# Kernel tuning notes

Hardware: AMD Instinct MI355X
Metric: run time of the kernel (lower is better)

## Reference

```python
import jax, jax.numpy as jnp
import numpy as np

N = 50000        # n_nodes
E = 800000       # n_edges (avg degree 16)
H = 64           # hidden_size
ALPHA = 0.5      # CRF alpha
BETA = 0.5       # CRF beta
N_LAYER = 2      # args.crf_layer
GAMMA = 0.2      # LeakyReLU negative slope


def setup_inputs() -> dict:
    key = jax.random.key(0)
    k = jax.random.split(key, 5)
    emb = jax.random.normal(k[0], (N, H), jnp.float32)
    W_fc = jax.random.normal(k[1], (H, H), jnp.float32) / np.sqrt(H)
    attn_fc_w = jax.random.normal(k[2], (1, 2 * H), jnp.float32) / np.sqrt(2 * H)
    src = jax.random.randint(k[3], (E,), 0, N, dtype=jnp.int32)
    dst = jax.random.randint(k[4], (E,), 0, N, dtype=jnp.int32)
    return {"emb": emb, "W_fc": W_fc, "attn_fc_w": attn_fc_w, "src": src, "dst": dst}


def _segment_softmax(e, dst, n):
    # softmax over incoming edges of each destination node (DGL mailbox softmax)
    m = jax.ops.segment_max(e, dst, num_segments=n)
    m = jnp.where(jnp.isfinite(m), m, 0.0)  # nodes with no in-edges
    ex = jnp.exp(e - m[dst])
    denom = jax.ops.segment_sum(ex, dst, num_segments=n)
    return ex / jnp.maximum(denom[dst], 1e-16)


def reference(emb, W_fc, attn_fc_w, src, dst):
    # attn_fc(concat(z_src, z_dst)) split into two per-node projections
    a_src = attn_fc_w[0, :H]
    a_dst = attn_fc_w[0, H:]
    h = emb
    e = None
    for _ in range(N_LAYER):
        z = h @ W_fc.T                              # [N, H] emb_attn
        e = (z @ a_src)[src] + (z @ a_dst)[dst]     # [E] edge logits
        e = jnp.where(e > 0, e, GAMMA * e)          # LeakyReLU(gamma)
        att = _segment_softmax(e, dst, N)           # [E]
        crf = jax.ops.segment_sum(att[:, None] * h[src], dst, num_segments=N)  # [N, H]
        h = (ALPHA * emb + BETA * crf) / (ALPHA + BETA)
    # training loss (is_train=True); reuses last layer's edge logits e
    loss_a = jnp.sum((h - emb) ** 2, axis=-1)                     # [N]
    att = _segment_softmax(e, dst, N)
    diff = jnp.sqrt(jnp.sum((h[dst] - h[src]) ** 2, axis=-1) + 1e-12)  # [E] L2 norm
    loss_b = jax.ops.segment_sum(att * diff, dst, num_segments=N)  # [N]
    loss = jnp.mean(ALPHA * loss_a + BETA * loss_b)
    return h, loss
```

## Files before the change

kernel.cpp:

```cpp
#include <hip/hip_runtime.h>

#define NNODES 50000
#define NEDGES 800000
#define HDIM 64
#define CAP 64
#define GAMMA 0.2f
#define INIT_B 256
#define INIT_NB ((NNODES + INIT_B - 1) / INIT_B)
#define NPART 8
#define NODES_PER_PART ((NNODES + NPART - 1) / NPART)
#define FILL_SLICES 192
#define E4 (NEDGES / 4)
#define CHUNK ((E4 + FILL_SLICES - 1) / FILL_SLICES)
#define NB ((NNODES + 3) / 4)

typedef unsigned short u16;
typedef unsigned int u32;

__device__ __forceinline__ u16 f2bf(float f) {
    u32 u = __float_as_uint(f);
    u32 r = (u + 0x7FFFu + ((u >> 16) & 1u)) >> 16;
    return (u16)r;
}
__device__ __forceinline__ float bflo(u32 u) { return __uint_as_float(u << 16); }
__device__ __forceinline__ float bfhi(u32 u) { return __uint_as_float(u & 0xFFFF0000u); }

__device__ __forceinline__ float wave_sum(float v) {
    #pragma unroll
    for (int off = 32; off; off >>= 1) v += __shfl_xor(v, off, 64);
    return v;
}
__device__ __forceinline__ float wave_max(float v) {
    #pragma unroll
    for (int off = 32; off; off >>= 1) v = fmaxf(v, __shfl_xor(v, off, 64));
    return v;
}
__device__ __forceinline__ float group8_sum(float v) {
    v += __shfl_xor(v, 1, 64);
    v += __shfl_xor(v, 2, 64);
    v += __shfl_xor(v, 4, 64);
    return v;
}

__global__ __launch_bounds__(256) void k_init(int* __restrict__ cursor,
                                              const float* __restrict__ Wfc,
                                              const float* __restrict__ attn,
                                              float* __restrict__ ws, float* __restrict__ wd) {
    int t = threadIdx.x;
    int idx = blockIdx.x * 256 + t;
    if (idx < NNODES) cursor[idx] = 0;
    if (blockIdx.x == gridDim.x - 1) {
        if (t >= 128) {
            int tt = t - 128;
            int k = tt & 63;
            const float* av = attn + ((tt >= 64) ? HDIM : 0);
            float s = 0.f;
            for (int j = 0; j < HDIM; ++j) s += Wfc[j * HDIM + k] * av[j];
            if (tt < 64) ws[k] = s; else wd[k] = s;
        }
    }
}

__global__ __launch_bounds__(256) void k_fillx(const int4* __restrict__ src4,
                                               const int4* __restrict__ dst4,
                                               int* __restrict__ cursor,
                                               u16* __restrict__ padded,
                                               const float* __restrict__ emb,
                                               const float* __restrict__ ws,
                                               const float* __restrict__ wd,
                                               u16* __restrict__ emb_bf,
                                               float* __restrict__ zs,
                                               float* __restrict__ zd) {
    const int part = blockIdx.x & (NPART - 1);
    const int slice = blockIdx.x >> 3;
    const int lo = slice * CHUNK;
    const int hi = min(lo + CHUNK, E4);
    const int plo = part * NODES_PER_PART;
    const int phi = plo + NODES_PER_PART;
    for (int i = lo + threadIdx.x; i < hi; i += 256) {
        int4 d = dst4[i];
        bool mx = d.x >= plo && d.x < phi;
        bool my = d.y >= plo && d.y < phi;
        bool mz = d.z >= plo && d.z < phi;
        bool mw = d.w >= plo && d.w < phi;
        if (mx | my | mz | mw) {
            int4 s = src4[i];
            if (mx) { int p0 = atomicAdd(&cursor[d.x], 1); if (p0 < CAP) padded[d.x * CAP + p0] = (u16)s.x; }
            if (my) { int p1 = atomicAdd(&cursor[d.y], 1); if (p1 < CAP) padded[d.y * CAP + p1] = (u16)s.y; }
            if (mz) { int p2 = atomicAdd(&cursor[d.z], 1); if (p2 < CAP) padded[d.z * CAP + p2] = (u16)s.z; }
            if (mw) { int p3 = atomicAdd(&cursor[d.w], 1); if (p3 < CAP) padded[d.w * CAP + p3] = (u16)s.w; }
        }
    }
    const int lane = threadIdx.x & 63;
    const int gw = (blockIdx.x * 256 + threadIdx.x) >> 6;
    const int nw = (gridDim.x * 256) >> 6;
    const float wsl = ws[lane], wdl = wd[lane];
    for (int n = gw; n < NNODES; n += nw) {
        float v = emb[n * HDIM + lane];
        emb_bf[n * HDIM + lane] = f2bf(v);
        float a = wave_sum(v * wsl);
        float b = wave_sum(v * wdl);
        if (lane == 0) { zs[n] = a; zd[n] = b; }
    }
}

template <bool COMPUTE_Z, bool WRITE_F32, bool STORE_LA>
__global__ __launch_bounds__(256) void k_layer(const u16* __restrict__ hbf_in,
                                               const float* __restrict__ emb,
                                               const int* __restrict__ deg,
                                               const u16* __restrict__ padded,
                                               const float* __restrict__ zs,
                                               const float* __restrict__ zd,
                                               float* __restrict__ h_out,
                                               u16* __restrict__ hbf_out,
                                               const float* __restrict__ ws,
                                               const float* __restrict__ wd,
                                               float* __restrict__ zs_out,
                                               float* __restrict__ zd_out,
                                               float* __restrict__ partialsA) {
    int wid = (blockIdx.x * blockDim.x + threadIdx.x) >> 6;
    int lane = threadIdx.x & 63;
    if (wid >= NNODES) return;
    int ne = min(deg[wid], CAP);
    float zdn = zd[wid];
    const int sub8 = lane >> 3, q8 = lane & 7;
    float acc[8];
    #pragma unroll
    for (int i = 0; i < 8; ++i) acc[i] = 0.f;

    int s = 0; float e = -INFINITY;
    bool valid = lane < ne;
    if (valid) {
        s = padded[(size_t)wid * CAP + lane];
        float z = zs[s] + zdn;
        e = z > 0.f ? z : GAMMA * z;
    }
    float m = wave_max(e);
    float ex = valid ? __expf(e - m) : 0.f;
    float dsum = wave_sum(ex);
    float inv = 1.f / fmaxf(dsum, 1e-16f);
    for (int j = 0; j < ne; j += 16) {
        int ja = j + sub8, jb = j + 8 + sub8;
        float wa = __shfl(ex, ja, 64);
        float wb = __shfl(ex, jb, 64);
        int ta = __shfl(s, ja, 64);
        int tb = __shfl(s, jb, 64);
        const uint4 ra = *(const uint4*)&hbf_in[(size_t)ta * HDIM + 8 * q8];
        const uint4 rb = *(const uint4*)&hbf_in[(size_t)tb * HDIM + 8 * q8];
        acc[0] += wa * bflo(ra.x) + wb * bflo(rb.x);
        acc[1] += wa * bfhi(ra.x) + wb * bfhi(rb.x);
        acc[2] += wa * bflo(ra.y) + wb * bflo(rb.y);
        acc[3] += wa * bfhi(ra.y) + wb * bfhi(rb.y);
        acc[4] += wa * bflo(ra.z) + wb * bflo(rb.z);
        acc[5] += wa * bfhi(ra.z) + wb * bfhi(rb.z);
        acc[6] += wa * bflo(ra.w) + wb * bflo(rb.w);
        acc[7] += wa * bfhi(ra.w) + wb * bfhi(rb.w);
    }
    #pragma unroll
    for (int off = 8; off <= 32; off <<= 1) {
        #pragma unroll
        for (int i = 0; i < 8; ++i) acc[i] += __shfl_xor(acc[i], off, 64);
    }
    float hv[8];
    #pragma unroll
    for (int i = 0; i < 8; ++i) hv[i] = 0.f;
    float lap = 0.f;
    if (sub8 == 0) {
        const float4 e0 = *(const float4*)&emb[(size_t)wid * HDIM + 8 * q8];
        const float4 e1 = *(const float4*)&emb[(size_t)wid * HDIM + 8 * q8 + 4];
        hv[0] = 0.5f * (e0.x + acc[0] * inv);
        hv[1] = 0.5f * (e0.y + acc[1] * inv);
        hv[2] = 0.5f * (e0.z + acc[2] * inv);
        hv[3] = 0.5f * (e0.w + acc[3] * inv);
        hv[4] = 0.5f * (e1.x + acc[4] * inv);
        hv[5] = 0.5f * (e1.y + acc[5] * inv);
        hv[6] = 0.5f * (e1.z + acc[6] * inv);
        hv[7] = 0.5f * (e1.w + acc[7] * inv);
        if (WRITE_F32) {
            *(float4*)&h_out[(size_t)wid * HDIM + 8 * q8]     = make_float4(hv[0], hv[1], hv[2], hv[3]);
            *(float4*)&h_out[(size_t)wid * HDIM + 8 * q8 + 4] = make_float4(hv[4], hv[5], hv[6], hv[7]);
        }
        uint4 o;
        o.x = (u32)f2bf(hv[0]) | ((u32)f2bf(hv[1]) << 16);
        o.y = (u32)f2bf(hv[2]) | ((u32)f2bf(hv[3]) << 16);
        o.z = (u32)f2bf(hv[4]) | ((u32)f2bf(hv[5]) << 16);
        o.w = (u32)f2bf(hv[6]) | ((u32)f2bf(hv[7]) << 16);
        *(uint4*)&hbf_out[(size_t)wid * HDIM + 8 * q8] = o;
        if (STORE_LA) {
            float d0 = hv[0] - e0.x, d1 = hv[1] - e0.y, d2 = hv[2] - e0.z, d3 = hv[3] - e0.w;
            float d4 = hv[4] - e1.x, d5 = hv[5] - e1.y, d6 = hv[6] - e1.z, d7 = hv[7] - e1.w;
            lap = d0 * d0 + d1 * d1 + d2 * d2 + d3 * d3 +
                  d4 * d4 + d5 * d5 + d6 * d6 + d7 * d7;
        }
    }
    if (STORE_LA) {
        float lsum = wave_sum(lap);
        __shared__ float ps[4];
        if (lane == 0) ps[threadIdx.x >> 6] = lsum;
        __syncthreads();
        if (threadIdx.x == 0)
            partialsA[blockIdx.x] = ps[0] + ps[1] + ps[2] + ps[3];
    }
    if (COMPUTE_Z) {
        float pa = 0.f, pb = 0.f;
        if (sub8 == 0) {
            const float4 w0 = *(const float4*)&ws[8 * q8];
            const float4 w1 = *(const float4*)&ws[8 * q8 + 4];
            const float4 d0 = *(const float4*)&wd[8 * q8];
            const float4 d1 = *(const float4*)&wd[8 * q8 + 4];
            pa = hv[0] * w0.x + hv[1] * w0.y + hv[2] * w0.z + hv[3] * w0.w +
                 hv[4] * w1.x + hv[5] * w1.y + hv[6] * w1.z + hv[7] * w1.w;
            pb = hv[0] * d0.x + hv[1] * d0.y + hv[2] * d0.z + hv[3] * d0.w +
                 hv[4] * d1.x + hv[5] * d1.y + hv[6] * d1.z + hv[7] * d1.w;
        }
        float a = wave_sum(pa);
        float b = wave_sum(pb);
        if (lane == 0) { zs_out[wid] = a; zd_out[wid] = b; }
    }
}

__global__ __launch_bounds__(256) void k_loss(const u16* __restrict__ hbf,
                                              const int* __restrict__ deg,
                                              const u16* __restrict__ padded,
                                              const float* __restrict__ zs,
                                              const float* __restrict__ zd,
                                              float* __restrict__ partialsB) {
    const int lane = threadIdx.x & 63;
    const int wib = threadIdx.x >> 6;
    const int wid = (blockIdx.x * blockDim.x + threadIdx.x) >> 6;
    const int sub8 = lane >> 3, q8 = lane & 7;
    float lb = 0.f;

    int ne = min(deg[wid], CAP);
    if (ne > 0) {
        const uint4 rd = *(const uint4*)&hbf[(size_t)wid * HDIM + 8 * q8];
        float zdn = zd[wid];
        int s = 0; float e = -INFINITY;
        bool valid = lane < ne;
        if (valid) {
            s = padded[(size_t)wid * CAP + lane];
            float z = zs[s] + zdn;
            e = z > 0.f ? z : GAMMA * z;
        }
        float m = wave_max(e);
        float ex = valid ? __expf(e - m) : 0.f;
        float dsum = wave_sum(ex);
        float att = ex * (1.f / fmaxf(dsum, 1e-16f));
        const float h0 = bflo(rd.x), h1 = bfhi(rd.x), h2 = bflo(rd.y), h3 = bfhi(rd.y);
        const float h4 = bflo(rd.z), h5 = bfhi(rd.z), h6 = bflo(rd.w), h7 = bfhi(rd.w);
        float part = 0.f;
        for (int j = 0; j < ne; j += 16) {
            int ja = j + sub8, jb = j + 8 + sub8;
            float wa = __shfl(att, ja, 64);
            float wb = __shfl(att, jb, 64);
            int ta = __shfl(s, ja, 64);
            int tb = __shfl(s, jb, 64);
            const uint4 ra = *(const uint4*)&hbf[(size_t)ta * HDIM + 8 * q8];
            const uint4 rb = *(const uint4*)&hbf[(size_t)tb * HDIM + 8 * q8];
            float a0 = bflo(ra.x) - h0, a1 = bfhi(ra.x) - h1;
            float a2 = bflo(ra.y) - h2, a3 = bfhi(ra.y) - h3;
            float a4 = bflo(ra.z) - h4, a5 = bfhi(ra.z) - h5;
            float a6 = bflo(ra.w) - h6, a7 = bfhi(ra.w) - h7;
            float b0 = bflo(rb.x) - h0, b1 = bfhi(rb.x) - h1;
            float b2 = bflo(rb.y) - h2, b3 = bfhi(rb.y) - h3;
            float b4 = bflo(rb.z) - h4, b5 = bfhi(rb.z) - h5;
            float b6 = bflo(rb.w) - h6, b7 = bfhi(rb.w) - h7;
            float ssa = group8_sum(a0 * a0 + a1 * a1 + a2 * a2 + a3 * a3 +
                                   a4 * a4 + a5 * a5 + a6 * a6 + a7 * a7);
            float ssb = group8_sum(b0 * b0 + b1 * b1 + b2 * b2 + b3 * b3 +
                                   b4 * b4 + b5 * b5 + b6 * b6 + b7 * b7);
            if (q8 == 0) part += wa * sqrtf(ssa + 1e-12f) + wb * sqrtf(ssb + 1e-12f);
        }
        lb = 0.5f * part;
    }
    lb = wave_sum(lb);
    __shared__ float psum[4];
    if (lane == 0) psum[wib] = lb;
    __syncthreads();
    if (threadIdx.x == 0)
        partialsB[blockIdx.x] = psum[0] + psum[1] + psum[2] + psum[3];
}

__global__ __launch_bounds__(256) void k_finalize(const float* __restrict__ partialsA,
                                                  const float* __restrict__ partialsB,
                                                  float* __restrict__ out_loss) {
    const int t = threadIdx.x;
    const int lane = t & 63;
    const int wib = t >> 6;
    float va = 0.f, vb = 0.f;
    for (int i = t; i < NB; i += 256) { va += partialsA[i]; vb += partialsB[i]; }
    float v = wave_sum(0.5f * va + vb);
    __shared__ float psum[4];
    if (lane == 0) psum[wib] = v;
    __syncthreads();
    if (t == 0) out_loss[0] = (psum[0] + psum[1] + psum[2] + psum[3]) / (float)NNODES;
}

extern "C" void kernel_launch(void* const* d_in, const int* in_sizes, int n_in,
                              void* d_out, int out_size, void* d_ws, size_t ws_size,
                              hipStream_t stream) {
    const float* emb  = (const float*)d_in[0];
    const float* Wfc  = (const float*)d_in[1];
    const float* attn = (const float*)d_in[2];
    const int*   src  = (const int*)d_in[3];
    const int*   dst  = (const int*)d_in[4];
    float* out = (float*)d_out;

    char* p = (char*)d_ws;
    int*   cursor   = (int*)p;   p += (size_t)NNODES * 4;
    float* wsv      = (float*)p; p += 64 * 4;
    float* wdv      = (float*)p; p += 64 * 4;
    float* zs0      = (float*)p; p += (size_t)NNODES * 4;
    float* zd0      = (float*)p; p += (size_t)NNODES * 4;
    float* zs1      = (float*)p; p += (size_t)NNODES * 4;
    float* zd1      = (float*)p; p += (size_t)NNODES * 4;
    float* partialsA= (float*)p; p += (size_t)NB * 4;
    float* partialsB= (float*)p; p += (size_t)NB * 4;
    p = (char*)(((size_t)p + 255) & ~(size_t)255);
    u16*   padded   = (u16*)p;   p += (size_t)NNODES * CAP * 2;
    u16*   emb_bf   = (u16*)p;   p += (size_t)NNODES * HDIM * 2;
    u16*   h1_bf    = (u16*)p;   p += (size_t)NNODES * HDIM * 2;
    u16*   out_bf   = (u16*)p;   p += (size_t)NNODES * HDIM * 2;

    k_init<<<INIT_NB, 256, 0, stream>>>(cursor, Wfc, attn, wsv, wdv);
    k_fillx<<<NPART * FILL_SLICES, 256, 0, stream>>>((const int4*)src, (const int4*)dst,
                                                     cursor, padded,
                                                     emb, wsv, wdv, emb_bf, zs0, zd0);

    k_layer<true, false, false><<<NB, 256, 0, stream>>>(
        emb_bf, emb, cursor, padded, zs0, zd0,
        out , h1_bf, wsv, wdv, zs1, zd1, partialsA);
    k_layer<false, true, true><<<NB, 256, 0, stream>>>(
        h1_bf, emb, cursor, padded, zs1, zd1,
        out, out_bf, wsv, wdv, zs0, zd0, partialsA);

    k_loss<<<NB, 256, 0, stream>>>(out_bf, cursor, padded, zs1, zd1, partialsB);
    k_finalize<<<1, 256, 0, stream>>>(partialsA, partialsB, out + (size_t)NNODES * HDIM);
}
```

Measured before the change: 225.2 us.

## Fuse all stages into one cooperative persistent kernel with grid syncs

Replaces the six separate kernel launches (init, CSR fill, two layers, loss, finalize) with a single cooperative kernel that runs each stage as a grid-stride phase separated by grid.sync(). The aim is to remove launch overhead and the inter-kernel gaps. In exchange the grid is capped at occupancy-limited size (at most 1024 blocks), so each phase loops over nodes, and the grid-wide barriers add their own cost. The grid size is computed once and cached in a static.

Measured after the change: 648.5 us. 188% more time.

```diff
diff --git a/kernel.cpp b/kernel.cpp
--- a/kernel.cpp
+++ b/kernel.cpp
@@ -1,17 +1,17 @@
 #include <hip/hip_runtime.h>
+#include <hip/hip_cooperative_groups.h>
+
+namespace cg = cooperative_groups;
 
 #define NNODES 50000
 #define NEDGES 800000
 #define HDIM 64
 #define CAP 64
 #define GAMMA 0.2f
-#define INIT_B 256
-#define INIT_NB ((NNODES + INIT_B - 1) / INIT_B)
 #define NPART 8
 #define NODES_PER_PART ((NNODES + NPART - 1) / NPART)
-#define FILL_SLICES 192
 #define E4 (NEDGES / 4)
-#define CHUNK ((E4 + FILL_SLICES - 1) / FILL_SLICES)
+#define MAX_GRID 1024
 #define NB ((NNODES + 3) / 4)
 
 typedef unsigned short u16;
@@ -42,197 +42,128 @@
     return v;
 }
 
-__global__ __launch_bounds__(256) void k_init(int* __restrict__ cursor,
-                                              const float* __restrict__ Wfc,
-                                              const float* __restrict__ attn,
-                                              float* __restrict__ ws, float* __restrict__ wd) {
-    int t = threadIdx.x;
-    int idx = blockIdx.x * 256 + t;
-    if (idx < NNODES) cursor[idx] = 0;
-    if (blockIdx.x == gridDim.x - 1) {
-        if (t >= 128) {
-            int tt = t - 128;
-            int k = tt & 63;
-            const float* av = attn + ((tt >= 64) ? HDIM : 0);
-            float s = 0.f;
-            for (int j = 0; j < HDIM; ++j) s += Wfc[j * HDIM + k] * av[j];
-            if (tt < 64) ws[k] = s; else wd[k] = s;
-        }
-    }
-}
-
-__global__ __launch_bounds__(256) void k_fillx(const int4* __restrict__ src4,
-                                               const int4* __restrict__ dst4,
-                                               int* __restrict__ cursor,
-                                               u16* __restrict__ padded,
-                                               const float* __restrict__ emb,
-                                               const float* __restrict__ ws,
-                                               const float* __restrict__ wd,
-                                               u16* __restrict__ emb_bf,
-                                               float* __restrict__ zs,
-                                               float* __restrict__ zd) {
-    const int part = blockIdx.x & (NPART - 1);
-    const int slice = blockIdx.x >> 3;
-    const int lo = slice * CHUNK;
-    const int hi = min(lo + CHUNK, E4);
-    const int plo = part * NODES_PER_PART;
-    const int phi = plo + NODES_PER_PART;
-    for (int i = lo + threadIdx.x; i < hi; i += 256) {
-        int4 d = dst4[i];
-        bool mx = d.x >= plo && d.x < phi;
-        bool my = d.y >= plo && d.y < phi;
-        bool mz = d.z >= plo && d.z < phi;
-        bool mw = d.w >= plo && d.w < phi;
-        if (mx | my | mz | mw) {
-            int4 s = src4[i];
-            if (mx) { int p0 = atomicAdd(&cursor[d.x], 1); if (p0 < CAP) padded[d.x * CAP + p0] = (u16)s.x; }
-            if (my) { int p1 = atomicAdd(&cursor[d.y], 1); if (p1 < CAP) padded[d.y * CAP + p1] = (u16)s.y; }
-            if (mz) { int p2 = atomicAdd(&cursor[d.z], 1); if (p2 < CAP) padded[d.z * CAP + p2] = (u16)s.z; }
-            if (mw) { int p3 = atomicAdd(&cursor[d.w], 1); if (p3 < CAP) padded[d.w * CAP + p3] = (u16)s.w; }
-        }
-    }
-    const int lane = threadIdx.x & 63;
-    const int gw = (blockIdx.x * 256 + threadIdx.x) >> 6;
-    const int nw = (gridDim.x * 256) >> 6;
-    const float wsl = ws[lane], wdl = wd[lane];
-    for (int n = gw; n < NNODES; n += nw) {
-        float v = emb[n * HDIM + lane];
-        emb_bf[n * HDIM + lane] = f2bf(v);
-        float a = wave_sum(v * wsl);
-        float b = wave_sum(v * wdl);
-        if (lane == 0) { zs[n] = a; zd[n] = b; }
-    }
-}
-
 template <bool COMPUTE_Z, bool WRITE_F32, bool STORE_LA>
-__global__ __launch_bounds__(256) void k_layer(const u16* __restrict__ hbf_in,
-                                               const float* __restrict__ emb,
-                                               const int* __restrict__ deg,
-                                               const u16* __restrict__ padded,
-                                               const float* __restrict__ zs,
-                                               const float* __restrict__ zd,
-                                               float* __restrict__ h_out,
-                                               u16* __restrict__ hbf_out,
-                                               const float* __restrict__ ws,
-                                               const float* __restrict__ wd,
-                                               float* __restrict__ zs_out,
-                                               float* __restrict__ zd_out,
-                                               float* __restrict__ partialsA) {
-    int wid = (blockIdx.x * blockDim.x + threadIdx.x) >> 6;
-    int lane = threadIdx.x & 63;
-    if (wid >= NNODES) return;
-    int ne = min(deg[wid], CAP);
-    float zdn = zd[wid];
-    const int sub8 = lane >> 3, q8 = lane & 7;
-    float acc[8];
-    #pragma unroll
-    for (int i = 0; i < 8; ++i) acc[i] = 0.f;
-
-    int s = 0; float e = -INFINITY;
-    bool valid = lane < ne;
-    if (valid) {
-        s = padded[(size_t)wid * CAP + lane];
-        float z = zs[s] + zdn;
-        e = z > 0.f ? z : GAMMA * z;
-    }
-    float m = wave_max(e);
-    float ex = valid ? __expf(e - m) : 0.f;
-    float dsum = wave_sum(ex);
-    float inv = 1.f / fmaxf(dsum, 1e-16f);
-    for (int j = 0; j < ne; j += 16) {
-        int ja = j + sub8, jb = j + 8 + sub8;
-        float wa = __shfl(ex, ja, 64);
-        float wb = __shfl(ex, jb, 64);
-        int ta = __shfl(s, ja, 64);
-        int tb = __shfl(s, jb, 64);
-        const uint4 ra = *(const uint4*)&hbf_in[(size_t)ta * HDIM + 8 * q8];
-        const uint4 rb = *(const uint4*)&hbf_in[(size_t)tb * HDIM + 8 * q8];
-        acc[0] += wa * bflo(ra.x) + wb * bflo(rb.x);
-        acc[1] += wa * bfhi(ra.x) + wb * bfhi(rb.x);
-        acc[2] += wa * bflo(ra.y) + wb * bflo(rb.y);
-        acc[3] += wa * bfhi(ra.y) + wb * bfhi(rb.y);
-        acc[4] += wa * bflo(ra.z) + wb * bflo(rb.z);
-        acc[5] += wa * bfhi(ra.z) + wb * bfhi(rb.z);
-        acc[6] += wa * bflo(ra.w) + wb * bflo(rb.w);
-        acc[7] += wa * bfhi(ra.w) + wb * bfhi(rb.w);
-    }
-    #pragma unroll
-    for (int off = 8; off <= 32; off <<= 1) {
-        #pragma unroll
-        for (int i = 0; i < 8; ++i) acc[i] += __shfl_xor(acc[i], off, 64);
-    }
-    float hv[8];
-    #pragma unroll
-    for (int i = 0; i < 8; ++i) hv[i] = 0.f;
-    float lap = 0.f;
-    if (sub8 == 0) {
-        const float4 e0 = *(const float4*)&emb[(size_t)wid * HDIM + 8 * q8];
-        const float4 e1 = *(const float4*)&emb[(size_t)wid * HDIM + 8 * q8 + 4];
-        hv[0] = 0.5f * (e0.x + acc[0] * inv);
-        hv[1] = 0.5f * (e0.y + acc[1] * inv);
-        hv[2] = 0.5f * (e0.z + acc[2] * inv);
-        hv[3] = 0.5f * (e0.w + acc[3] * inv);
-        hv[4] = 0.5f * (e1.x + acc[4] * inv);
-        hv[5] = 0.5f * (e1.y + acc[5] * inv);
-        hv[6] = 0.5f * (e1.z + acc[6] * inv);
-        hv[7] = 0.5f * (e1.w + acc[7] * inv);
-        if (WRITE_F32) {
-            *(float4*)&h_out[(size_t)wid * HDIM + 8 * q8]     = make_float4(hv[0], hv[1], hv[2], hv[3]);
-            *(float4*)&h_out[(size_t)wid * HDIM + 8 * q8 + 4] = make_float4(hv[4], hv[5], hv[6], hv[7]);
-        }
-        uint4 o;
-        o.x = (u32)f2bf(hv[0]) | ((u32)f2bf(hv[1]) << 16);
-        o.y = (u32)f2bf(hv[2]) | ((u32)f2bf(hv[3]) << 16);
-        o.z = (u32)f2bf(hv[4]) | ((u32)f2bf(hv[5]) << 16);
-        o.w = (u32)f2bf(hv[6]) | ((u32)f2bf(hv[7]) << 16);
-        *(uint4*)&hbf_out[(size_t)wid * HDIM + 8 * q8] = o;
-        if (STORE_LA) {
-            float d0 = hv[0] - e0.x, d1 = hv[1] - e0.y, d2 = hv[2] - e0.z, d3 = hv[3] - e0.w;
-            float d4 = hv[4] - e1.x, d5 = hv[5] - e1.y, d6 = hv[6] - e1.z, d7 = hv[7] - e1.w;
-            lap = d0 * d0 + d1 * d1 + d2 * d2 + d3 * d3 +
-                  d4 * d4 + d5 * d5 + d6 * d6 + d7 * d7;
-        }
-    }
-    if (STORE_LA) {
-        float lsum = wave_sum(lap);
-        __shared__ float ps[4];
-        if (lane == 0) ps[threadIdx.x >> 6] = lsum;
-        __syncthreads();
-        if (threadIdx.x == 0)
-            partialsA[blockIdx.x] = ps[0] + ps[1] + ps[2] + ps[3];
-    }
-    if (COMPUTE_Z) {
-        float pa = 0.f, pb = 0.f;
-        if (sub8 == 0) {
-            const float4 w0 = *(const float4*)&ws[8 * q8];
-            const float4 w1 = *(const float4*)&ws[8 * q8 + 4];
-            const float4 d0 = *(const float4*)&wd[8 * q8];
-            const float4 d1 = *(const float4*)&wd[8 * q8 + 4];
-            pa = hv[0] * w0.x + hv[1] * w0.y + hv[2] * w0.z + hv[3] * w0.w +
-                 hv[4] * w1.x + hv[5] * w1.y + hv[6] * w1.z + hv[7] * w1.w;
-            pb = hv[0] * d0.x + hv[1] * d0.y + hv[2] * d0.z + hv[3] * d0.w +
-                 hv[4] * d1.x + hv[5] * d1.y + hv[6] * d1.z + hv[7] * d1.w;
-        }
-        float a = wave_sum(pa);
-        float b = wave_sum(pb);
-        if (lane == 0) { zs_out[wid] = a; zd_out[wid] = b; }
-    }
-}
-
-__global__ __launch_bounds__(256) void k_loss(const u16* __restrict__ hbf,
-                                              const int* __restrict__ deg,
-                                              const u16* __restrict__ padded,
-                                              const float* __restrict__ zs,
-                                              const float* __restrict__ zd,
-                                              float* __restrict__ partialsB) {
+__device__ __forceinline__ float layer_phase(const u16* __restrict__ hbf_in,
+                                             const float* __restrict__ emb,
+                                             const int* __restrict__ deg,
+                                             const u16* __restrict__ padded,
+                                             const float* __restrict__ zs,
+                                             const float* __restrict__ zd,
+                                             float* __restrict__ h_out,
+                                             u16* __restrict__ hbf_out,
+                                             const float* __restrict__ ws,
+                                             const float* __restrict__ wd,
+                                             float* __restrict__ zs_out,
+                                             float* __restrict__ zd_out) {
     const int lane = threadIdx.x & 63;
     const int wib = threadIdx.x >> 6;
-    const int wid = (blockIdx.x * blockDim.x + threadIdx.x) >> 6;
     const int sub8 = lane >> 3, q8 = lane & 7;
-    float lb = 0.f;
-
-    int ne = min(deg[wid], CAP);
-    if (ne > 0) {
+    float laAcc = 0.f;
+    for (int g = blockIdx.x; g < NB; g += gridDim.x) {
+        const int wid = g * 4 + wib;
+        int ne = min(deg[wid], CAP);
+        float zdn = zd[wid];
+        float acc[8];
+        #pragma unroll
+        for (int i = 0; i < 8; ++i) acc[i] = 0.f;
+
+        int s = 0; float e = -INFINITY;
+        bool valid = lane < ne;
+        if (valid) {
+            s = padded[(size_t)wid * CAP + lane];
+            float z = zs[s] + zdn;
+            e = z > 0.f ? z : GAMMA * z;
+        }
+        float m = wave_max(e);
+        float ex = valid ? __expf(e - m) : 0.f;
+        float dsum = wave_sum(ex);
+        float inv = 1.f / fmaxf(dsum, 1e-16f);
+        for (int j = 0; j < ne; j += 16) {
+            int ja = j + sub8, jb = j + 8 + sub8;
+            float wa = __shfl(ex, ja, 64);
+            float wb = __shfl(ex, jb, 64);
+            int ta = __shfl(s, ja, 64);
+            int tb = __shfl(s, jb, 64);
+            const uint4 ra = *(const uint4*)&hbf_in[(size_t)ta * HDIM + 8 * q8];
+            const uint4 rb = *(const uint4*)&hbf_in[(size_t)tb * HDIM + 8 * q8];
+            acc[0] += wa * bflo(ra.x) + wb * bflo(rb.x);
+            acc[1] += wa * bfhi(ra.x) + wb * bfhi(rb.x);
+            acc[2] += wa * bflo(ra.y) + wb * bflo(rb.y);
+            acc[3] += wa * bfhi(ra.y) + wb * bfhi(rb.y);
+            acc[4] += wa * bflo(ra.z) + wb * bflo(rb.z);
+            acc[5] += wa * bfhi(ra.z) + wb * bfhi(rb.z);
+            acc[6] += wa * bflo(ra.w) + wb * bflo(rb.w);
+            acc[7] += wa * bfhi(ra.w) + wb * bfhi(rb.w);
+        }
+        #pragma unroll
+        for (int off = 8; off <= 32; off <<= 1) {
+            #pragma unroll
+            for (int i = 0; i < 8; ++i) acc[i] += __shfl_xor(acc[i], off, 64);
+        }
+        float hv[8];
+        #pragma unroll
+        for (int i = 0; i < 8; ++i) hv[i] = 0.f;
+        if (sub8 == 0) {
+            const float4 e0 = *(const float4*)&emb[(size_t)wid * HDIM + 8 * q8];
+            const float4 e1 = *(const float4*)&emb[(size_t)wid * HDIM + 8 * q8 + 4];
+            hv[0] = 0.5f * (e0.x + acc[0] * inv);
+            hv[1] = 0.5f * (e0.y + acc[1] * inv);
+            hv[2] = 0.5f * (e0.z + acc[2] * inv);
+            hv[3] = 0.5f * (e0.w + acc[3] * inv);
+            hv[4] = 0.5f * (e1.x + acc[4] * inv);
+            hv[5] = 0.5f * (e1.y + acc[5] * inv);
+            hv[6] = 0.5f * (e1.z + acc[6] * inv);
+            hv[7] = 0.5f * (e1.w + acc[7] * inv);
+            if (WRITE_F32) {
+                *(float4*)&h_out[(size_t)wid * HDIM + 8 * q8]     = make_float4(hv[0], hv[1], hv[2], hv[3]);
+                *(float4*)&h_out[(size_t)wid * HDIM + 8 * q8 + 4] = make_float4(hv[4], hv[5], hv[6], hv[7]);
+            }
+            uint4 o;
+            o.x = (u32)f2bf(hv[0]) | ((u32)f2bf(hv[1]) << 16);
+            o.y = (u32)f2bf(hv[2]) | ((u32)f2bf(hv[3]) << 16);
+            o.z = (u32)f2bf(hv[4]) | ((u32)f2bf(hv[5]) << 16);
+            o.w = (u32)f2bf(hv[6]) | ((u32)f2bf(hv[7]) << 16);
+            *(uint4*)&hbf_out[(size_t)wid * HDIM + 8 * q8] = o;
+            if (STORE_LA) {
+                float d0 = hv[0] - e0.x, d1 = hv[1] - e0.y, d2 = hv[2] - e0.z, d3 = hv[3] - e0.w;
+                float d4 = hv[4] - e1.x, d5 = hv[5] - e1.y, d6 = hv[6] - e1.z, d7 = hv[7] - e1.w;
+                laAcc += d0 * d0 + d1 * d1 + d2 * d2 + d3 * d3 +
+                         d4 * d4 + d5 * d5 + d6 * d6 + d7 * d7;
+            }
+        }
+        if (COMPUTE_Z) {
+            float pa = 0.f, pb = 0.f;
+            if (sub8 == 0) {
+                const float4 w0 = *(const float4*)&ws[8 * q8];
+                const float4 w1 = *(const float4*)&ws[8 * q8 + 4];
+                const float4 d0 = *(const float4*)&wd[8 * q8];
+                const float4 d1 = *(const float4*)&wd[8 * q8 + 4];
+                pa = hv[0] * w0.x + hv[1] * w0.y + hv[2] * w0.z + hv[3] * w0.w +
+                     hv[4] * w1.x + hv[5] * w1.y + hv[6] * w1.z + hv[7] * w1.w;
+                pb = hv[0] * d0.x + hv[1] * d0.y + hv[2] * d0.z + hv[3] * d0.w +
+                     hv[4] * d1.x + hv[5] * d1.y + hv[6] * d1.z + hv[7] * d1.w;
+            }
+            float a = wave_sum(pa);
+            float b = wave_sum(pb);
+            if (lane == 0) { zs_out[wid] = a; zd_out[wid] = b; }
+        }
+    }
+    return laAcc;
+}
+
+__device__ __forceinline__ float loss_phase(const u16* __restrict__ hbf,
+                                            const int* __restrict__ deg,
+                                            const u16* __restrict__ padded,
+                                            const float* __restrict__ zs,
+                                            const float* __restrict__ zd) {
+    const int lane = threadIdx.x & 63;
+    const int wib = threadIdx.x >> 6;
+    const int sub8 = lane >> 3, q8 = lane & 7;
+    float lbAcc = 0.f;
+    for (int g = blockIdx.x; g < NB; g += gridDim.x) {
+        const int wid = g * 4 + wib;
+        int ne = min(deg[wid], CAP);
+        if (ne == 0) continue;
         const uint4 rd = *(const uint4*)&hbf[(size_t)wid * HDIM + 8 * q8];
         float zdn = zd[wid];
         int s = 0; float e = -INFINITY;
@@ -271,29 +202,111 @@
                                    b4 * b4 + b5 * b5 + b6 * b6 + b7 * b7);
             if (q8 == 0) part += wa * sqrtf(ssa + 1e-12f) + wb * sqrtf(ssb + 1e-12f);
         }
-        lb = 0.5f * part;
-    }
-    lb = wave_sum(lb);
-    __shared__ float psum[4];
-    if (lane == 0) psum[wib] = lb;
-    __syncthreads();
-    if (threadIdx.x == 0)
-        partialsB[blockIdx.x] = psum[0] + psum[1] + psum[2] + psum[3];
-}
-
-__global__ __launch_bounds__(256) void k_finalize(const float* __restrict__ partialsA,
-                                                  const float* __restrict__ partialsB,
-                                                  float* __restrict__ out_loss) {
+        lbAcc += 0.5f * part;
+    }
+    return lbAcc;
+}
+
+__global__ __launch_bounds__(256, 4) void k_mega(
+    const int4* __restrict__ src4, const int4* __restrict__ dst4,
+    int* __restrict__ cursor, u16* __restrict__ padded,
+    const float* __restrict__ emb, const float* __restrict__ Wfc,
+    const float* __restrict__ attn,
+    float* __restrict__ ws, float* __restrict__ wd,
+    u16* __restrict__ emb_bf, float* __restrict__ zs0, float* __restrict__ zd0,
+    float* __restrict__ zs1, float* __restrict__ zd1,
+    u16* __restrict__ h1_bf, u16* __restrict__ out_bf,
+    float* __restrict__ h_out,
+    float* __restrict__ partialsA, float* __restrict__ partialsB,
+    float* __restrict__ out_loss) {
+    cg::grid_group grid = cg::this_grid();
     const int t = threadIdx.x;
+    const int bid = blockIdx.x;
+    const int nblk = gridDim.x;
     const int lane = t & 63;
     const int wib = t >> 6;
-    float va = 0.f, vb = 0.f;
-    for (int i = t; i < NB; i += 256) { va += partialsA[i]; vb += partialsB[i]; }
-    float v = wave_sum(0.5f * va + vb);
-    __shared__ float psum[4];
-    if (lane == 0) psum[wib] = v;
-    __syncthreads();
-    if (t == 0) out_loss[0] = (psum[0] + psum[1] + psum[2] + psum[3]) / (float)NNODES;
+    __shared__ float ps[4];
+
+    {
+        for (int idx = bid * 256 + t; idx < NNODES; idx += nblk * 256) cursor[idx] = 0;
+        if (bid == 0 && t >= 128) {
+            int tt = t - 128;
+            int k = tt & 63;
+            const float* av = attn + ((tt >= 64) ? HDIM : 0);
+            float s = 0.f;
+            for (int j = 0; j < HDIM; ++j) s += Wfc[j * HDIM + k] * av[j];
+            if (tt < 64) ws[k] = s; else wd[k] = s;
+        }
+    }
+    grid.sync();
+
+    {
+        const int part = bid & (NPART - 1);
+        const int slice = bid >> 3;
+        const int slices = nblk >> 3;
+        const int chunk = (E4 + slices - 1) / slices;
+        const int lo = slice * chunk;
+        const int hi = min(lo + chunk, E4);
+        const int plo = part * NODES_PER_PART;
+        const int phi = plo + NODES_PER_PART;
+        for (int i = lo + t; i < hi; i += 256) {
+            int4 d = dst4[i];
+            bool mx = d.x >= plo && d.x < phi;
+            bool my = d.y >= plo && d.y < phi;
+            bool mz = d.z >= plo && d.z < phi;
+            bool mw = d.w >= plo && d.w < phi;
+            if (mx | my | mz | mw) {
+                int4 s = src4[i];
+                if (mx) { int p = atomicAdd(&cursor[d.x], 1); if (p < CAP) padded[d.x * CAP + p] = (u16)s.x; }
+                if (my) { int p = atomicAdd(&cursor[d.y], 1); if (p < CAP) padded[d.y * CAP + p] = (u16)s.y; }
+                if (mz) { int p = atomicAdd(&cursor[d.z], 1); if (p < CAP) padded[d.z * CAP + p] = (u16)s.z; }
+                if (mw) { int p = atomicAdd(&cursor[d.w], 1); if (p < CAP) padded[d.w * CAP + p] = (u16)s.w; }
+            }
+        }
+        const int gw = (bid * 256 + t) >> 6;
+        const int nw = nblk * 4;
+        const float wsl = ws[lane], wdl = wd[lane];
+        for (int n = gw; n < NNODES; n += nw) {
+            float v = emb[n * HDIM + lane];
+            emb_bf[n * HDIM + lane] = f2bf(v);
+            float a = wave_sum(v * wsl);
+            float b = wave_sum(v * wdl);
+            if (lane == 0) { zs0[n] = a; zd0[n] = b; }
+        }
+    }
+    grid.sync();
+
+    layer_phase<true, false, false>(emb_bf, emb, cursor, padded, zs0, zd0,
+                                    h_out , h1_bf, ws, wd, zs1, zd1);
+    grid.sync();
+
+    {
+        float la = layer_phase<false, true, true>(h1_bf, emb, cursor, padded, zs1, zd1,
+                                                  h_out, out_bf, ws, wd, zs0, zd0);
+        la = wave_sum(la);
+        if (lane == 0) ps[wib] = la;
+        __syncthreads();
+        if (t == 0) partialsA[bid] = ps[0] + ps[1] + ps[2] + ps[3];
+    }
+    grid.sync();
+
+    {
+        float lb = loss_phase(out_bf, cursor, padded, zs1, zd1);
+        lb = wave_sum(lb);
+        if (lane == 0) ps[wib] = lb;
+        __syncthreads();
+        if (t == 0) partialsB[bid] = ps[0] + ps[1] + ps[2] + ps[3];
+    }
+    grid.sync();
+
+    if (bid == 0) {
+        float va = 0.f, vb = 0.f;
+        for (int i = t; i < nblk; i += 256) { va += partialsA[i]; vb += partialsB[i]; }
+        float v = wave_sum(0.5f * va + vb);
+        if (lane == 0) ps[wib] = v;
+        __syncthreads();
+        if (t == 0) out_loss[0] = (ps[0] + ps[1] + ps[2] + ps[3]) / (float)NNODES;
+    }
 }
 
 extern "C" void kernel_launch(void* const* d_in, const int* in_sizes, int n_in,
@@ -302,8 +315,8 @@
     const float* emb  = (const float*)d_in[0];
     const float* Wfc  = (const float*)d_in[1];
     const float* attn = (const float*)d_in[2];
-    const int*   src  = (const int*)d_in[3];
-    const int*   dst  = (const int*)d_in[4];
+    const int4*  src4 = (const int4*)d_in[3];
+    const int4*  dst4 = (const int4*)d_in[4];
     float* out = (float*)d_out;
 
     char* p = (char*)d_ws;
@@ -314,26 +327,39 @@
     float* zd0      = (float*)p; p += (size_t)NNODES * 4;
     float* zs1      = (float*)p; p += (size_t)NNODES * 4;
     float* zd1      = (float*)p; p += (size_t)NNODES * 4;
-    float* partialsA= (float*)p; p += (size_t)NB * 4;
-    float* partialsB= (float*)p; p += (size_t)NB * 4;
+    float* partialsA= (float*)p; p += (size_t)MAX_GRID * 4;
+    float* partialsB= (float*)p; p += (size_t)MAX_GRID * 4;
     p = (char*)(((size_t)p + 255) & ~(size_t)255);
     u16*   padded   = (u16*)p;   p += (size_t)NNODES * CAP * 2;
     u16*   emb_bf   = (u16*)p;   p += (size_t)NNODES * HDIM * 2;
     u16*   h1_bf    = (u16*)p;   p += (size_t)NNODES * HDIM * 2;
     u16*   out_bf   = (u16*)p;   p += (size_t)NNODES * HDIM * 2;
 
-    k_init<<<INIT_NB, 256, 0, stream>>>(cursor, Wfc, attn, wsv, wdv);
-    k_fillx<<<NPART * FILL_SLICES, 256, 0, stream>>>((const int4*)src, (const int4*)dst,
-                                                     cursor, padded,
-                                                     emb, wsv, wdv, emb_bf, zs0, zd0);
-
-    k_layer<true, false, false><<<NB, 256, 0, stream>>>(
-        emb_bf, emb, cursor, padded, zs0, zd0,
-        out , h1_bf, wsv, wdv, zs1, zd1, partialsA);
-    k_layer<false, true, true><<<NB, 256, 0, stream>>>(
-        h1_bf, emb, cursor, padded, zs1, zd1,
-        out, out_bf, wsv, wdv, zs0, zd0, partialsA);
-
-    k_loss<<<NB, 256, 0, stream>>>(out_bf, cursor, padded, zs1, zd1, partialsB);
-    k_finalize<<<1, 256, 0, stream>>>(partialsA, partialsB, out + (size_t)NNODES * HDIM);
-}
+    float* out_loss = out + (size_t)NNODES * HDIM;
+
+    static int gridBlks = 0;
+    if (gridBlks == 0) {
+        int mb = 0;
+        if (hipOccupancyMaxActiveBlocksPerMultiprocessor(&mb, k_mega, 256, 0) != hipSuccess || mb < 1)
+            mb = 1;
+        int g = mb * 256;
+        if (g > MAX_GRID) g = MAX_GRID;
+        g &= ~7;
+        if (g < 8) g = 8;
+        gridBlks = g;
+    }
+
+    void* args[] = {
+        (void*)&src4, (void*)&dst4, (void*)&cursor, (void*)&padded,
+        (void*)&emb, (void*)&Wfc, (void*)&attn,
+        (void*)&wsv, (void*)&wdv,
+        (void*)&emb_bf, (void*)&zs0, (void*)&zd0,
+        (void*)&zs1, (void*)&zd1,
+        (void*)&h1_bf, (void*)&out_bf,
+        (void*)&out,
+        (void*)&partialsA, (void*)&partialsB,
+        (void*)&out_loss
+    };
+    hipLaunchCooperativeKernel((const void*)k_mega, dim3(gridBlks), dim3(256),
+                               args, 0, stream);
+}
```
